# Optimization experiments

Hardware: AMD Instinct MI355X
Metric: run time of the kernel (lower is better)

Reference implementation:

```python
import jax, jax.numpy as jnp
import numpy as np

B = 4096
D = 1024
N = 100000
KS = (10000, 20000, 50000)


def _l2norm(x):
    # F.normalize(p=2, dim=1, eps=1e-12): x / max(||x||, eps)
    n = jnp.sqrt(jnp.sum(x * x, axis=1, keepdims=True))
    return x / jnp.maximum(n, 1e-12)


def setup_inputs() -> dict:
    key = jax.random.key(0)
    ks = jax.random.split(key, 16)
    inp = {}
    inp["anchor"] = jax.random.normal(ks[0], (B, D), jnp.float32)
    inp["index"] = jax.random.randint(ks[1], (B,), 0, N)
    for i, K in enumerate(KS):
        inp[f"inst2cluster{i}"] = jax.random.randint(ks[2 + i], (N,), 0, K)
        inp[f"centroids{i}"] = jax.random.normal(ks[5 + i], (K, D), jnp.float32)
        # density acts as a per-column temperature; keep it bounded away from 0
        inp[f"density{i}"] = jax.random.uniform(ks[8 + i], (K,), jnp.float32, 0.1, 1.0)
    return inp


def reference(anchor, centroids0, centroids1, centroids2,
              density0, density1, density2,
              index, inst2cluster0, inst2cluster1, inst2cluster2):
    Bn = anchor.shape[0]
    a = _l2norm(anchor)
    rows = jnp.arange(Bn)
    cols = jnp.arange(Bn - 1)
    # negatives[i, j] = sim[i, j + (j >= i)] -> row i without its diagonal entry
    neg_idx = cols[None, :] + (cols[None, :] >= rows[:, None])  # [B, B-1]

    scales = [(inst2cluster0, centroids0, density0),
              (inst2cluster1, centroids1, density1),
              (inst2cluster2, centroids2, density2)]
    n_scales = len(scales)

    loss = jnp.zeros(Bn, anchor.dtype)
    for i2c, cent, dens in scales:
        protos = _l2norm(cent)
        pos_id = i2c[index]                       # [B]
        sim = a @ protos[pos_id].T                # [B, B]
        pos = jnp.diagonal(sim)[:, None]          # [B, 1]
        neg = jnp.take_along_axis(sim, neg_idx, axis=1)  # [B, B-1]
        # torch broadcast: [B, B] / [B] divides column j by temp_proto[j]
        logits = jnp.concatenate([pos, neg], axis=1) / dens[pos_id][None, :]
        # CE with label 0, reduction='none'
        ce = jax.nn.logsumexp(logits, axis=1) - logits[:, 0]
        # faithful to the original: division by len(cluster_result) INSIDE the loop
        loss = (loss + ce) / n_scales
    return loss
```

## Files before the change

### kernel.cpp

```cpp
#include <hip/hip_runtime.h>

#define BB 4096
#define DD 1024
#define RTS (BB + 16)
#define BK 32
#define NT (DD / BK)

typedef float f32x4 __attribute__((ext_vector_type(4)));
typedef short bf16x8 __attribute__((ext_vector_type(8)));

__device__ __forceinline__ unsigned short f2bf(float f) {
  unsigned u = __float_as_uint(f);
  unsigned r = u + 0x7fffu + ((u >> 16) & 1u);
  return (unsigned short)(r >> 16);
}

__device__ __forceinline__ void async16(const void* g, void* l) {
  __builtin_amdgcn_global_load_lds(
      (const __attribute__((address_space(1))) void*)g,
      (__attribute__((address_space(3))) void*)l,
      16, 0, 0);
}

__global__ __launch_bounds__(256) void norm_anchor(const float* __restrict__ x,
                                                   unsigned short* __restrict__ y) {
  __shared__ float sred[4];
  const int row = blockIdx.x;
  const int tid = threadIdx.x;
  const float4 v = ((const float4*)(x + (size_t)row * DD))[tid];
  float ss = v.x * v.x + v.y * v.y + v.z * v.z + v.w * v.w;
#pragma unroll
  for (int off = 32; off > 0; off >>= 1) ss += __shfl_xor(ss, off, 64);
  if ((tid & 63) == 0) sred[tid >> 6] = ss;
  __syncthreads();
  const float tot = sred[0] + sred[1] + sred[2] + sred[3];
  const float inv = 1.0f / fmaxf(sqrtf(tot), 1e-12f);
  ushort4 o;
  o.x = f2bf(v.x * inv);
  o.y = f2bf(v.y * inv);
  o.z = f2bf(v.z * inv);
  o.w = f2bf(v.w * inv);
  ((ushort4*)(y + (size_t)row * DD))[tid] = o;
}

__global__ __launch_bounds__(256) void gather_norm(
    const int* __restrict__ index,
    const int* __restrict__ i2c0, const int* __restrict__ i2c1, const int* __restrict__ i2c2,
    const float* __restrict__ c0, const float* __restrict__ c1, const float* __restrict__ c2,
    const float* __restrict__ d0, const float* __restrict__ d1, const float* __restrict__ d2,
    unsigned short* __restrict__ p16, float* __restrict__ rt,
    float* __restrict__ rowacc) {
  __shared__ float sred[4];
  const int j = blockIdx.x;
  const int s = blockIdx.y;
  const int tid = threadIdx.x;
  const int* i2c = (s == 0) ? i2c0 : (s == 1) ? i2c1 : i2c2;
  const float* cent = (s == 0) ? c0 : (s == 1) ? c1 : c2;
  const float* dens = (s == 0) ? d0 : (s == 1) ? d1 : d2;
  const int pid = i2c[index[j]];
  const float4 v = ((const float4*)(cent + (size_t)pid * DD))[tid];
  float ss = v.x * v.x + v.y * v.y + v.z * v.z + v.w * v.w;
#pragma unroll
  for (int off = 32; off > 0; off >>= 1) ss += __shfl_xor(ss, off, 64);
  if ((tid & 63) == 0) sred[tid >> 6] = ss;
  __syncthreads();
  const float tot = sred[0] + sred[1] + sred[2] + sred[3];
  const float inv = 1.0f / fmaxf(sqrtf(tot), 1e-12f);
  unsigned short* out = p16 + ((size_t)s * BB + j) * DD;
  ushort4 o;
  o.x = f2bf(v.x * inv);
  o.y = f2bf(v.y * inv);
  o.z = f2bf(v.z * inv);
  o.w = f2bf(v.w * inv);
  ((ushort4*)out)[tid] = o;
  if (tid == 0) rt[(size_t)s * RTS + j] = 1.0f / dens[pid];
  if (tid == 1) rowacc[(size_t)s * BB + j] = 0.0f;
}

__global__ __launch_bounds__(512, 2) void gemm_ce_fused(const unsigned short* __restrict__ A,
                                                        const unsigned short* __restrict__ P,
                                                        const float* __restrict__ rt,
                                                        float* __restrict__ rowacc,
                                                        float* __restrict__ diag) {
  __shared__ __align__(16) unsigned short smem[4][2][16][512];
  __shared__ float rsum[256][4];
  const int tid = threadIdx.x;
  const int lane = tid & 63;
  const int wave = tid >> 6;
  const int wm = wave >> 2;
  const int wn = wave & 3;
  const int m0 = blockIdx.y * 256;
  const int n0 = blockIdx.x * 256;
  const int s = blockIdx.z;
  const unsigned short* Bm = P + (size_t)s * BB * DD;
  const float* rt_s = rt + (size_t)s * RTS;

  const int row_l = lane >> 2;
  const int col_e = (((lane & 3) ^ ((row_l >> 1) & 3)) << 3);
  const int SA = wave * 2;
  const unsigned short* gA0 = A + (size_t)(m0 + SA * 16 + row_l) * DD + col_e;
  const unsigned short* gA1 = gA0 + (size_t)16 * DD;
  const unsigned short* gB0 = Bm + (size_t)(n0 + SA * 16 + row_l) * DD + col_e;
  const unsigned short* gB1 = gB0 + (size_t)16 * DD;

#define STAGE4(bb)                                   \
  do {                                               \
    async16(gA0, &smem[bb][0][SA][0]);               \
    async16(gA1, &smem[bb][0][SA + 1][0]);           \
    async16(gB0, &smem[bb][1][SA][0]);               \
    async16(gB1, &smem[bb][1][SA + 1][0]);           \
    gA0 += BK; gA1 += BK; gB0 += BK; gB1 += BK;      \
  } while (0)

  STAGE4(0);
  STAGE4(1);
  STAGE4(2);

  const int fr = lane & 15;
  const int fq = lane >> 4;
  const int aoff = fr * 32 + ((fq ^ ((fr >> 1) & 3)) << 3);

  f32x4 acc[8][4];
#pragma unroll
  for (int mi = 0; mi < 8; ++mi)
#pragma unroll
    for (int ni = 0; ni < 4; ++ni) acc[mi][ni] = (f32x4){0.f, 0.f, 0.f, 0.f};

  for (int t = 0; t < NT; ++t) {
    if (t < NT - 2)       asm volatile("s_waitcnt vmcnt(8) lgkmcnt(0)" ::: "memory");
    else if (t == NT - 2) asm volatile("s_waitcnt vmcnt(4) lgkmcnt(0)" ::: "memory");
    else                  asm volatile("s_waitcnt vmcnt(0) lgkmcnt(0)" ::: "memory");
    __builtin_amdgcn_s_barrier();

    const int b = t & 3;
    if (t < NT - 3) STAGE4((t + 3) & 3);

    bf16x8 bv[4];
#pragma unroll
    for (int ni = 0; ni < 4; ++ni)
      bv[ni] = *(const bf16x8*)(&smem[b][1][wn * 4 + ni][0] + aoff);
#pragma unroll
    for (int mi = 0; mi < 8; ++mi) {
      const bf16x8 af = *(const bf16x8*)(&smem[b][0][wm * 8 + mi][0] + aoff);
#pragma unroll
      for (int ni = 0; ni < 4; ++ni)
        acc[mi][ni] = __builtin_amdgcn_mfma_f32_16x16x32_bf16(af, bv[ni], acc[mi][ni], 0, 0, 0);
    }
  }
#undef STAGE4

  const int cm = fq * 4;
  const float rt0 = rt_s[0];
  float rtc[4], rtp[4];
#pragma unroll
  for (int ni = 0; ni < 4; ++ni) {
    const int col = n0 + wn * 64 + ni * 16 + fr;
    rtc[ni] = rt_s[col];
    rtp[ni] = rt_s[col + 1];
  }
#pragma unroll
  for (int mi = 0; mi < 8; ++mi) {
#pragma unroll
    for (int r = 0; r < 4; ++r) {
      const int rowi = m0 + wm * 128 + mi * 16 + cm + r;
      float esum = 0.f;
#pragma unroll
      for (int ni = 0; ni < 4; ++ni) {
        const int col = n0 + wn * 64 + ni * 16 + fr;
        const float v = acc[mi][ni][r];
        const float rr = (col == rowi) ? rt0 : ((col < rowi) ? rtp[ni] : rtc[ni]);
        const float l = v * rr;
        if (col == rowi) diag[(size_t)s * BB + rowi] = l;
        esum += __expf(l);
      }
#pragma unroll
      for (int off = 1; off < 16; off <<= 1) esum += __shfl_xor(esum, off, 64);
      if (fr == 0) rsum[wm * 128 + mi * 16 + cm + r][wn] = esum;
    }
  }
  __syncthreads();
  if (tid < 256) {
    const float v = rsum[tid][0] + rsum[tid][1] + rsum[tid][2] + rsum[tid][3];
    atomicAdd(&rowacc[(size_t)s * BB + m0 + tid], v);
  }
}

__global__ __launch_bounds__(256) void finish(const float* __restrict__ rowacc,
                                              const float* __restrict__ diag,
                                              float* __restrict__ out) {
  const int i = blockIdx.x * 256 + threadIdx.x;
  const float ce0 = logf(rowacc[i]) - diag[i];
  const float ce1 = logf(rowacc[BB + i]) - diag[BB + i];
  const float ce2 = logf(rowacc[2 * BB + i]) - diag[2 * BB + i];
  out[i] = ce0 * (1.0f / 27.0f) + ce1 * (1.0f / 9.0f) + ce2 * (1.0f / 3.0f);
}

extern "C" void kernel_launch(void* const* d_in, const int* in_sizes, int n_in,
                              void* d_out, int out_size, void* d_ws, size_t ws_size,
                              hipStream_t stream) {
  const float* anchor = (const float*)d_in[0];
  const int* index    = (const int*)d_in[1];
  const int* i2c0     = (const int*)d_in[2];
  const float* c0     = (const float*)d_in[3];
  const float* de0    = (const float*)d_in[4];
  const int* i2c1     = (const int*)d_in[5];
  const float* c1     = (const float*)d_in[6];
  const float* de1    = (const float*)d_in[7];
  const int* i2c2     = (const int*)d_in[8];
  const float* c2     = (const float*)d_in[9];
  const float* de2    = (const float*)d_in[10];

  char* ws = (char*)d_ws;
  const size_t A16_OFF = 0;
  const size_t P16_OFF = A16_OFF + (size_t)BB * DD * 2;
  const size_t RT_OFF  = P16_OFF + (size_t)3 * BB * DD * 2;
  const size_t ACC_OFF = RT_OFF + (size_t)3 * RTS * 4;
  const size_t DIA_OFF = ACC_OFF + (size_t)3 * BB * 4;

  unsigned short* a16 = (unsigned short*)(ws + A16_OFF);
  unsigned short* p16 = (unsigned short*)(ws + P16_OFF);
  float* rt     = (float*)(ws + RT_OFF);
  float* rowacc = (float*)(ws + ACC_OFF);
  float* diag   = (float*)(ws + DIA_OFF);
  float* out = (float*)d_out;

  norm_anchor<<<BB, 256, 0, stream>>>(anchor, a16);
  gather_norm<<<dim3(BB, 3), 256, 0, stream>>>(index, i2c0, i2c1, i2c2,
                                               c0, c1, c2, de0, de1, de2, p16, rt, rowacc);
  gemm_ce_fused<<<dim3(BB / 256, BB / 256, 3), 512, 0, stream>>>(a16, p16, rt, rowacc, diag);
  finish<<<BB / 256, 256, 0, stream>>>(rowacc, diag, out);
}
```

Measured before the change: 452.6 us.

## Shrink fused GEMM-CE tile to 128x128 with 4 waves and 3-stage pipeline

The fused GEMM+CE kernel moves from 256x256 output tiles with 8 waves and a 4-deep LDS ring to 128x128 tiles with 4 waves and a 3-deep ring. Each wave now keeps a 64x64 accumulator instead of 128x64, which cuts register pressure and raises the occupancy target to 3 blocks per CU. The grid grows from 768 to 3072 blocks, giving better load balance across CUs. In exchange, each block reuses less data per tile, so global/L2 traffic doubles, and the shallower prefetch depth may expose more load latency.

Result: no change. 444.3 us (-1.8%).

```diff
diff --git a/kernel.cpp b/kernel.cpp
--- a/kernel.cpp
+++ b/kernel.cpp
@@ -77,20 +77,19 @@
   if (tid == 1) rowacc[(size_t)s * BB + j] = 0.0f;
 }
 
-__global__ __launch_bounds__(512, 2) void gemm_ce_fused(const unsigned short* __restrict__ A,
+__global__ __launch_bounds__(256, 3) void gemm_ce_fused(const unsigned short* __restrict__ A,
                                                         const unsigned short* __restrict__ P,
                                                         const float* __restrict__ rt,
                                                         float* __restrict__ rowacc,
                                                         float* __restrict__ diag) {
-  __shared__ __align__(16) unsigned short smem[4][2][16][512];
-  __shared__ float rsum[256][4];
+  __shared__ __align__(16) unsigned short lA[3][8][512];
+  __shared__ __align__(16) unsigned short lB[3][8][512];
+  __shared__ float rowsum[2][128];
   const int tid = threadIdx.x;
   const int lane = tid & 63;
   const int wave = tid >> 6;
-  const int wm = wave >> 2;
-  const int wn = wave & 3;
-  const int m0 = blockIdx.y * 256;
-  const int n0 = blockIdx.x * 256;
+  const int m0 = blockIdx.y * 128;
+  const int n0 = blockIdx.x * 128;
   const int s = blockIdx.z;
   const unsigned short* Bm = P + (size_t)s * BB * DD;
   const float* rt_s = rt + (size_t)s * RTS;
@@ -103,70 +102,75 @@
   const unsigned short* gB0 = Bm + (size_t)(n0 + SA * 16 + row_l) * DD + col_e;
   const unsigned short* gB1 = gB0 + (size_t)16 * DD;
 
-#define STAGE4(bb)                                   \
-  do {                                               \
-    async16(gA0, &smem[bb][0][SA][0]);               \
-    async16(gA1, &smem[bb][0][SA + 1][0]);           \
-    async16(gB0, &smem[bb][1][SA][0]);               \
-    async16(gB1, &smem[bb][1][SA + 1][0]);           \
-    gA0 += BK; gA1 += BK; gB0 += BK; gB1 += BK;      \
+#define STAGE4(bb)                               \
+  do {                                           \
+    async16(gA0, &lA[bb][SA][0]);                \
+    async16(gA1, &lA[bb][SA + 1][0]);            \
+    async16(gB0, &lB[bb][SA][0]);                \
+    async16(gB1, &lB[bb][SA + 1][0]);            \
+    gA0 += BK; gA1 += BK; gB0 += BK; gB1 += BK;  \
   } while (0)
 
   STAGE4(0);
   STAGE4(1);
-  STAGE4(2);
 
   const int fr = lane & 15;
   const int fq = lane >> 4;
   const int aoff = fr * 32 + ((fq ^ ((fr >> 1) & 3)) << 3);
-
-  f32x4 acc[8][4];
-#pragma unroll
-  for (int mi = 0; mi < 8; ++mi)
+  const int wm = wave >> 1;
+  const int wn = wave & 1;
+
+  f32x4 acc[4][4];
+#pragma unroll
+  for (int mi = 0; mi < 4; ++mi)
 #pragma unroll
     for (int ni = 0; ni < 4; ++ni) acc[mi][ni] = (f32x4){0.f, 0.f, 0.f, 0.f};
 
+  int bt = 0;
+  int bs = 2;
   for (int t = 0; t < NT; ++t) {
-    if (t < NT - 2)       asm volatile("s_waitcnt vmcnt(8) lgkmcnt(0)" ::: "memory");
-    else if (t == NT - 2) asm volatile("s_waitcnt vmcnt(4) lgkmcnt(0)" ::: "memory");
-    else                  asm volatile("s_waitcnt vmcnt(0) lgkmcnt(0)" ::: "memory");
+    if (t < NT - 1) asm volatile("s_waitcnt vmcnt(4)" ::: "memory");
+    else            asm volatile("s_waitcnt vmcnt(0)" ::: "memory");
     __builtin_amdgcn_s_barrier();
 
-    const int b = t & 3;
-    if (t < NT - 3) STAGE4((t + 3) & 3);
+    if (t < NT - 2) STAGE4(bs);
 
     bf16x8 bv[4];
 #pragma unroll
     for (int ni = 0; ni < 4; ++ni)
-      bv[ni] = *(const bf16x8*)(&smem[b][1][wn * 4 + ni][0] + aoff);
-#pragma unroll
-    for (int mi = 0; mi < 8; ++mi) {
-      const bf16x8 af = *(const bf16x8*)(&smem[b][0][wm * 8 + mi][0] + aoff);
+      bv[ni] = *(const bf16x8*)(&lB[bt][wn * 4 + ni][0] + aoff);
+#pragma unroll
+    for (int mi = 0; mi < 4; ++mi) {
+      const bf16x8 af = *(const bf16x8*)(&lA[bt][wm * 4 + mi][0] + aoff);
 #pragma unroll
       for (int ni = 0; ni < 4; ++ni)
         acc[mi][ni] = __builtin_amdgcn_mfma_f32_16x16x32_bf16(af, bv[ni], acc[mi][ni], 0, 0, 0);
     }
+    bt = (bt == 2) ? 0 : bt + 1;
+    bs = (bs == 2) ? 0 : bs + 1;
   }
 #undef STAGE4
 
+  const int WMO = wm * 64;
+  const int WNO = wn * 64;
   const int cm = fq * 4;
   const float rt0 = rt_s[0];
   float rtc[4], rtp[4];
 #pragma unroll
   for (int ni = 0; ni < 4; ++ni) {
-    const int col = n0 + wn * 64 + ni * 16 + fr;
+    const int col = n0 + WNO + ni * 16 + fr;
     rtc[ni] = rt_s[col];
     rtp[ni] = rt_s[col + 1];
   }
 #pragma unroll
-  for (int mi = 0; mi < 8; ++mi) {
+  for (int mi = 0; mi < 4; ++mi) {
 #pragma unroll
     for (int r = 0; r < 4; ++r) {
-      const int rowi = m0 + wm * 128 + mi * 16 + cm + r;
+      const int rowi = m0 + WMO + mi * 16 + cm + r;
       float esum = 0.f;
 #pragma unroll
       for (int ni = 0; ni < 4; ++ni) {
-        const int col = n0 + wn * 64 + ni * 16 + fr;
+        const int col = n0 + WNO + ni * 16 + fr;
         const float v = acc[mi][ni][r];
         const float rr = (col == rowi) ? rt0 : ((col < rowi) ? rtp[ni] : rtc[ni]);
         const float l = v * rr;
@@ -175,14 +179,12 @@
       }
 #pragma unroll
       for (int off = 1; off < 16; off <<= 1) esum += __shfl_xor(esum, off, 64);
-      if (fr == 0) rsum[wm * 128 + mi * 16 + cm + r][wn] = esum;
+      if (fr == 0) rowsum[wn][WMO + mi * 16 + cm + r] = esum;
     }
   }
   __syncthreads();
-  if (tid < 256) {
-    const float v = rsum[tid][0] + rsum[tid][1] + rsum[tid][2] + rsum[tid][3];
-    atomicAdd(&rowacc[(size_t)s * BB + m0 + tid], v);
-  }
+  if (tid < 128)
+    atomicAdd(&rowacc[(size_t)s * BB + m0 + tid], rowsum[0][tid] + rowsum[1][tid]);
 }
 
 __global__ __launch_bounds__(256) void finish(const float* __restrict__ rowacc,
@@ -227,6 +229,6 @@
   norm_anchor<<<BB, 256, 0, stream>>>(anchor, a16);
   gather_norm<<<dim3(BB, 3), 256, 0, stream>>>(index, i2c0, i2c1, i2c2,
                                                c0, c1, c2, de0, de1, de2, p16, rt, rowacc);
-  gemm_ce_fused<<<dim3(BB / 256, BB / 256, 3), 512, 0, stream>>>(a16, p16, rt, rowacc, diag);
+  gemm_ce_fused<<<dim3(BB / 128, BB / 128, 3), 256, 0, stream>>>(a16, p16, rt, rowacc, diag);
   finish<<<BB / 256, 256, 0, stream>>>(rowacc, diag, out);
 }
```
